# Kernel tuning notes

Measured on AMD Instinct MI355X. Metric: run time of the kernel, lower is better.

Reference implementation:

```python
import jax, jax.numpy as jnp
import numpy as np
import math

NUM_BUCKETS = 32
MAX_DISTANCE = 128
N_HEADS = 16
D_KV = 64


def _relative_position_bucket(relative_position, num_buckets=NUM_BUCKETS, max_distance=MAX_DISTANCE):
    # bidirectional (encoder) variant: is_decoder=False
    nb = num_buckets // 2
    rel_buckets = (relative_position > 0).astype(jnp.int32) * nb
    rp = jnp.abs(relative_position)
    max_exact = nb // 2
    is_small = rp < max_exact
    rp_large = max_exact + (
        jnp.log(rp.astype(jnp.float32) / max_exact)
        / math.log(max_distance / max_exact)
        * (nb - max_exact)
    ).astype(jnp.int32)
    rp_large = jnp.minimum(rp_large, nb - 1)
    return rel_buckets + jnp.where(is_small, rp, rp_large)


def compute_position_bias(rel_bias_table, q_len, k_len):
    ctx = jnp.arange(q_len, dtype=jnp.int32)[:, None]
    mem = jnp.arange(k_len, dtype=jnp.int32)[None, :]
    buckets = _relative_position_bucket(mem - ctx)  # [q_len, k_len]
    values = rel_bias_table[buckets]                # [q_len, k_len, H]
    return jnp.transpose(values, (2, 0, 1))[None]   # [1, H, q_len, k_len]


def setup_inputs() -> dict:
    key = jax.random.key(0)
    ks = jax.random.split(key, 6)
    B, S, D = 2, 2048, 1024
    s = 0.02
    return {
        "hidden_states": jax.random.normal(ks[0], (B, S, D), dtype=jnp.float32),
        "Wq": jax.random.normal(ks[1], (D, N_HEADS * D_KV), dtype=jnp.float32) * s,
        "Wk": jax.random.normal(ks[2], (D, N_HEADS * D_KV), dtype=jnp.float32) * s,
        "Wv": jax.random.normal(ks[3], (D, N_HEADS * D_KV), dtype=jnp.float32) * s,
        "Wo": jax.random.normal(ks[4], (N_HEADS * D_KV, D), dtype=jnp.float32) * s,
        "rel_bias_table": jax.random.normal(ks[5], (NUM_BUCKETS, N_HEADS), dtype=jnp.float32),
    }


def reference(hidden_states, Wq, Wk, Wv, Wo, rel_bias_table):
    B, S, D = hidden_states.shape
    H, dh = N_HEADS, D_KV
    q = (hidden_states @ Wq).reshape(B, S, H, dh)
    k = (hidden_states @ Wk).reshape(B, S, H, dh)
    v = (hidden_states @ Wv).reshape(B, S, H, dh)

    position_bias = compute_position_bias(rel_bias_table, S, S)  # [1,H,S,S]

    scale = 1.0 / math.sqrt(dh)  # applied inside optimized_attention (SDPA convention)
    scores = jnp.einsum('bqhd,bkhd->bhqk', q, k) * scale + position_bias
    probs = jax.nn.softmax(scores, axis=-1)
    ctx = jnp.einsum('bhqk,bkhd->bqhd', probs, v).reshape(B, S, H * dh)
    attn_output = ctx @ Wo
    return attn_output
```

## Files before the change

### kernel.cpp

```cpp
#include <hip/hip_runtime.h>

typedef __attribute__((ext_vector_type(8))) short s16x8;
typedef __attribute__((ext_vector_type(4))) short s16x4;
typedef __attribute__((ext_vector_type(4))) float f32x4;
typedef __attribute__((ext_vector_type(4))) unsigned int u32x4;
typedef __attribute__((ext_vector_type(2))) unsigned int u32x2;
typedef unsigned short u16;
typedef unsigned int u32;

#define LOG2E 1.4426950408889634f

__device__ __forceinline__ u16 f2bf(float x) {
  u32 u = __float_as_uint(x);
  u += 0x7FFFu + ((u >> 16) & 1u);
  return (u16)(u >> 16);
}

__device__ __forceinline__ float bf2f(u16 x) {
  return __uint_as_float((u32)x << 16);
}

__device__ __forceinline__ u32 pack_bf_trunc(float lo, float hi) {
  return (__float_as_uint(lo) >> 16) | (__float_as_uint(hi) & 0xFFFF0000u);
}

__device__ __forceinline__ void gl_lds16(const void* g, void* l) {
  __builtin_amdgcn_global_load_lds((const __attribute__((address_space(1))) void*)g,
                                   (__attribute__((address_space(3))) void*)l, 16, 0, 0);
}

#define MFMA16(a, b, c) __builtin_amdgcn_mfma_f32_16x16x32_bf16((a), (b), (c), 0, 0, 0)


__global__ __launch_bounds__(256) void prep(const float* __restrict__ hs,
                                            const float* __restrict__ Wq,
                                            const float* __restrict__ Wk,
                                            const float* __restrict__ Wv,
                                            const float* __restrict__ Wo,
                                            const float* __restrict__ tbl,
                                            u16* __restrict__ hsb,
                                            u16* __restrict__ wt,
                                            u16* __restrict__ wot,
                                            float* __restrict__ biasT) {
  const int blk = blockIdx.x;
  const int tid = threadIdx.x;
  if (blk < 2048) {
    const int i = blk * 256 + tid;
    const float4* s4 = (const float4*)hs;
    float4 a = s4[i * 2];
    float4 b = s4[i * 2 + 1];
    s16x8 o;
    o[0] = (short)f2bf(a.x); o[1] = (short)f2bf(a.y);
    o[2] = (short)f2bf(a.z); o[3] = (short)f2bf(a.w);
    o[4] = (short)f2bf(b.x); o[5] = (short)f2bf(b.y);
    o[6] = (short)f2bf(b.z); o[7] = (short)f2bf(b.w);
    *(s16x8*)&hsb[i * 8] = o;
  } else if (blk < 4096) {
    int r = blk - 2048;
    const int sel = r >> 9;
    r &= 511;
    const float* W = sel == 0 ? Wq : (sel == 1 ? Wk : (sel == 2 ? Wv : Wo));
    u16* dst = sel == 3 ? wot : wt + sel * 1048576;
    const int n = (r & 15) * 64 + (tid & 63);
    const int kb = (r >> 4) * 32 + (tid >> 6) * 8;
    s16x8 o;
#pragma unroll
    for (int j = 0; j < 8; ++j) o[j] = (short)f2bf(W[(kb + j) * 1024 + n]);
    *(s16x8*)&dst[n * 1024 + kb] = o;
  } else {
    const int i = (blk - 4096) * 256 + tid;
    const int h = i >> 12, dp = i & 4095;
    const int delta = dp - 2047;
    const int rp = delta < 0 ? -delta : delta;
    int bucket = delta > 0 ? 16 : 0;
    if (rp < 8)
      bucket += rp;
    else
      bucket += 8 + (rp >= 12) + (rp >= 16) + (rp >= 23) + (rp >= 32) +
                (rp >= 46) + (rp >= 64) + (rp >= 91);
    biasT[i] = tbl[bucket * 16 + h] * LOG2E;
  }
}


__device__ __forceinline__ void gemm_core(const u16* __restrict__ A,
                                          const u16* __restrict__ Bt,
                                          int m0, int n0,
                                          u16* As, u16* Bs, f32x4 acc[4][4]) {
  const int tid = threadIdx.x;
  const int w = tid >> 6, l = tid & 63, g = l >> 4, m15 = l & 15;
  const int wr = (w >> 1) * 64, wc = (w & 1) * 64;
#pragma unroll
  for (int i = 0; i < 4; ++i)
#pragma unroll
    for (int j = 0; j < 4; ++j) acc[i][j] = (f32x4){0.f, 0.f, 0.f, 0.f};

  for (int kt = 0; kt < 16; ++kt) {
    const int k0 = kt * 64;
    __syncthreads();
#pragma unroll
    for (int c = 0; c < 4; ++c) {
      const int idx = c * 256 + tid;
      const int row = idx >> 3, col16 = idx & 7;
      const int scol = col16 ^ (row & 7);
      gl_lds16(&A[(m0 + row) * 1024 + k0 + scol * 8], (char*)As + c * 4096 + w * 1024);
      gl_lds16(&Bt[(n0 + row) * 1024 + k0 + scol * 8], (char*)Bs + c * 4096 + w * 1024);
    }
    __syncthreads();
#pragma unroll
    for (int ks = 0; ks < 2; ++ks) {
      s16x8 af[4], bf[4];
#pragma unroll
      for (int mf = 0; mf < 4; ++mf) {
        const int row = wr + mf * 16 + m15;
        af[mf] = *(const s16x8*)&As[(row * 8 + ((ks * 4 + g) ^ (row & 7))) * 8];
      }
#pragma unroll
      for (int nf = 0; nf < 4; ++nf) {
        const int row = wc + nf * 16 + m15;
        bf[nf] = *(const s16x8*)&Bs[(row * 8 + ((ks * 4 + g) ^ (row & 7))) * 8];
      }
#pragma unroll
      for (int mf = 0; mf < 4; ++mf)
#pragma unroll
        for (int nf = 0; nf < 4; ++nf)
          acc[mf][nf] = MFMA16(af[mf], bf[nf], acc[mf][nf]);
    }
  }
}

__global__ __launch_bounds__(256) void gemm_qkv(const u16* __restrict__ X,
                                                const u16* __restrict__ Wt,
                                                u16* __restrict__ Q,
                                                u16* __restrict__ Kb,
                                                u16* __restrict__ VT) {
  __shared__ u16 shbuf[16384];
  u16* As = shbuf;
  u16* Bs = shbuf + 8192;
  f32x4 acc[4][4];
  const int flat = blockIdx.x;
  const int x = flat & 7, i = flat >> 3;
  const int m0 = ((x & 3) * 8 + (i & 7)) * 128;
  const int n0 = ((x >> 2) * 12 + (i >> 3)) * 128;
  gemm_core(X, Wt, m0, n0, As, Bs, acc);

  const int tid = threadIdx.x;
  const int w = tid >> 6, l = tid & 63, g = l >> 4, m15 = l & 15;
  const int wr = (w >> 1) * 64, wc = (w & 1) * 64;
  const int nsel = n0 >> 10;
  const int ncol0 = (n0 & 1023) + wc;
  if (nsel == 2) {
    __syncthreads();
#pragma unroll
    for (int mf = 0; mf < 4; ++mf) {
      const int s_base = wr + mf * 16 + g * 4;
#pragma unroll
      for (int nf = 0; nf < 4; ++nf) {
        const int d_loc = wc + nf * 16 + m15;
        s16x4 pk;
#pragma unroll
        for (int r = 0; r < 4; ++r) pk[r] = (short)f2bf(acc[mf][nf][r]);
        *(s16x4*)&shbuf[d_loc * 128 + (s_base ^ ((d_loc & 7) << 3))] = pk;
      }
    }
    __syncthreads();
    const int b = m0 >> 11, sg0 = m0 & 2047;
#pragma unroll
    for (int it = 0; it < 8; ++it) {
      const int d_loc = it * 16 + w * 4 + g;
      const s16x8 v =
          *(const s16x8*)&shbuf[d_loc * 128 + ((m15 * 8) ^ ((d_loc & 7) << 3))];
      const int col = (n0 & 1023) + d_loc;
      *(s16x8*)&VT[((b * 16 + (col >> 6)) * 64 + (col & 63)) * 2048 + sg0 + m15 * 8] = v;
    }
  } else {
    u16* dst = nsel == 0 ? Q : Kb;
    const float scale = nsel == 0 ? 0.125f * LOG2E : 1.0f;
#pragma unroll
    for (int mf = 0; mf < 4; ++mf) {
      const int rbase = m0 + wr + mf * 16 + g * 4;
#pragma unroll
      for (int nf = 0; nf < 4; ++nf) {
        const int col = ncol0 + nf * 16 + m15;
#pragma unroll
        for (int r = 0; r < 4; ++r)
          dst[(rbase + r) * 1024 + col] = f2bf(acc[mf][nf][r] * scale);
      }
    }
  }
}

__global__ __launch_bounds__(256) void gemm_out(const u16* __restrict__ CTX,
                                                const u16* __restrict__ Wot,
                                                float* __restrict__ Out) {
  __shared__ u16 shbuf[16384];
  u16* As = shbuf;
  u16* Bs = shbuf + 8192;
  f32x4 acc[4][4];
  const int flat = blockIdx.x;
  const int x = flat & 7, i = flat >> 3;
  const int m0 = ((x & 3) * 8 + (i & 7)) * 128;
  const int n0 = ((x >> 2) * 4 + (i >> 3)) * 128;
  gemm_core(CTX, Wot, m0, n0, As, Bs, acc);

  const int tid = threadIdx.x;
  const int w = tid >> 6, l = tid & 63, g = l >> 4, m15 = l & 15;
  const int wr = (w >> 1) * 64, wc = (w & 1) * 64;
#pragma unroll
  for (int mf = 0; mf < 4; ++mf) {
    const int rbase = m0 + wr + mf * 16 + g * 4;
#pragma unroll
    for (int nf = 0; nf < 4; ++nf) {
      const int col = n0 + wc + nf * 16 + m15;
#pragma unroll
      for (int r = 0; r < 4; ++r)
        Out[(rbase + r) * 1024 + col] = acc[mf][nf][r];
    }
  }
}


__global__ __launch_bounds__(256, 4) void attn_kernel(const u16* __restrict__ Qg,
                                                      const u16* __restrict__ Kg,
                                                      const u16* __restrict__ VTg,
                                                      const float* __restrict__ biasT,
                                                      const float* __restrict__ tbl,
                                                      u16* __restrict__ po0,
                                                      u16* __restrict__ po1,
                                                      float* __restrict__ pls) {
  __shared__ u16 KT[2][4096];
  __shared__ u16 VTs[2][4096];

  const int tid = threadIdx.x;
  const int w = tid >> 6, l = tid & 63, g = l >> 4, m15 = l & 15;
  const int flat = blockIdx.x;
  const int nf_ = (flat & 7) * 128 + (flat >> 3);
  const int bh = nf_ >> 5;
  const int rem = nf_ & 31;
  const int half = rem >> 4, qblk = rem & 15;
  const int b = bh >> 4, h = bh & 15;
  const int qw = qblk * 128 + w * 32;
  const int kvbase = half * 1024;

  u16* poh = half ? po1 : po0;
  float* plsh = pls + half * 65536;

  const float fpos = tbl[31 * 16 + h] * LOG2E;
  const float fneg = tbl[15 * 16 + h] * LOG2E;

  s16x8 aq[2][2];
#pragma unroll
  for (int qs = 0; qs < 2; ++qs) {
    const u16* qp = &Qg[(b * 2048 + qw + qs * 16 + m15) * 1024 + h * 64 + g * 8];
    aq[qs][0] = *(const s16x8*)qp;
    aq[qs][1] = *(const s16x8*)(qp + 32);
  }

  s16x8 vone;
#pragma unroll
  for (int j = 0; j < 8; ++j) vone[j] = (short)0x3F80;

  f32x4 o[2][4];
  f32x4 ls4[2];
#pragma unroll
  for (int qs = 0; qs < 2; ++qs) {
    ls4[qs] = (f32x4){0.f, 0.f, 0.f, 0.f};
#pragma unroll
    for (int d = 0; d < 4; ++d) o[qs][d] = (f32x4){0.f, 0.f, 0.f, 0.f};
  }

  const u16* Kbase = &Kg[(b * 2048 + kvbase) * 1024 + h * 64];
  const u16* Vbase = &VTg[bh * 64 * 2048 + kvbase];

#define STAGE(buf, kv0)                                                          \
  {                                                                              \
    _Pragma("unroll") for (int c = 0; c < 2; ++c) {                              \
      const int idx = c * 256 + tid;                                             \
      const int row = idx >> 3, col16 = idx & 7;                                 \
      const int scol = col16 ^ (row & 7);                                        \
      gl_lds16(&Kbase[(kv0 + row) * 1024 + scol * 8],                            \
               (char*)KT + (buf)*8192 + c * 4096 + w * 1024);                    \
      gl_lds16(&Vbase[row * 2048 + (kv0) + scol * 8],                            \
               (char*)VTs + (buf)*8192 + c * 4096 + w * 1024);                   \
    }                                                                            \
  }

  STAGE(0, 0);
  int cur = 0;
  for (int t = 0; t < 16; ++t) {
    const int kv0 = t * 64;
    __syncthreads();
    if (t < 15) STAGE(cur ^ 1, kv0 + 64);

    const u16* KTc = &KT[cur][0];
    const u16* VTc = &VTs[cur][0];

    f32x4 s[2][4];
    const int diff = kvbase + kv0 - qw;
    if (diff <= -160 || diff >= 128) {
      const float bc = diff > 0 ? fpos : fneg;
#pragma unroll
      for (int qs = 0; qs < 2; ++qs)
#pragma unroll
        for (int c = 0; c < 4; ++c) s[qs][c] = (f32x4){bc, bc, bc, bc};
    } else {
#pragma unroll
      for (int qs = 0; qs < 2; ++qs) {
        const float* bp =
            &biasT[h * 4096 + kvbase + kv0 + g * 4 - qw - qs * 16 - m15 + 2047];
#pragma unroll
        for (int c = 0; c < 4; ++c)
#pragma unroll
          for (int r = 0; r < 4; ++r) s[qs][c][r] = bp[c * 16 + r];
      }
    }

    __builtin_amdgcn_s_setprio(1);
#pragma unroll
    for (int ks = 0; ks < 2; ++ks) {
#pragma unroll
      for (int c = 0; c < 4; ++c) {
        const int row = c * 16 + m15;
        const s16x8 bk = *(const s16x8*)&KTc[(row * 8 + ((ks * 4 + g) ^ (row & 7))) * 8];
        s[0][c] = MFMA16(bk, aq[0][ks], s[0][c]);
        s[1][c] = MFMA16(bk, aq[1][ks], s[1][c]);
      }
    }
    __builtin_amdgcn_s_setprio(0);

    s16x8 pa[2][2];
#pragma unroll
    for (int qs = 0; qs < 2; ++qs) {
      u32 w01[4], w23[4];
#pragma unroll
      for (int c = 0; c < 4; ++c) {
        w01[c] = pack_bf_trunc(__builtin_amdgcn_exp2f(s[qs][c][0]),
                               __builtin_amdgcn_exp2f(s[qs][c][1]));
        w23[c] = pack_bf_trunc(__builtin_amdgcn_exp2f(s[qs][c][2]),
                               __builtin_amdgcn_exp2f(s[qs][c][3]));
      }
#pragma unroll
      for (int ks = 0; ks < 2; ++ks) {
        u32x2 rA = __builtin_amdgcn_permlane32_swap(w01[2 * ks], w01[2 * ks + 1], false, false);
        u32x2 rB = __builtin_amdgcn_permlane16_swap(rA[0], rA[1], false, false);
        u32x2 rC = __builtin_amdgcn_permlane32_swap(w23[2 * ks], w23[2 * ks + 1], false, false);
        u32x2 rD = __builtin_amdgcn_permlane16_swap(rC[0], rC[1], false, false);
        const u32x4 pd = (u32x4){rB[0], rD[0], rB[1], rD[1]};
        pa[qs][ks] = __builtin_bit_cast(s16x8, pd);
      }
    }

    __builtin_amdgcn_s_setprio(1);
#pragma unroll
    for (int ks = 0; ks < 2; ++ks) {
#pragma unroll
      for (int d = 0; d < 4; ++d) {
        const int rowv = d * 16 + m15;
        const s16x8 bv = *(const s16x8*)&VTc[(rowv * 8 + ((ks * 4 + g) ^ (rowv & 7))) * 8];
        o[0][d] = MFMA16(pa[0][ks], bv, o[0][d]);
        o[1][d] = MFMA16(pa[1][ks], bv, o[1][d]);
      }
      ls4[0] = MFMA16(pa[0][ks], vone, ls4[0]);
      ls4[1] = MFMA16(pa[1][ks], vone, ls4[1]);
    }
    __builtin_amdgcn_s_setprio(0);
    cur ^= 1;
  }
#undef STAGE

#pragma unroll
  for (int qs = 0; qs < 2; ++qs) {
    const int orow = b * 2048 + qw + qs * 16 + g * 4;
    const int ocol = h * 64 + m15;
#pragma unroll
    for (int r = 0; r < 4; ++r) {
#pragma unroll
      for (int d = 0; d < 4; ++d)
        poh[(orow + r) * 1024 + ocol + d * 16] = f2bf(o[qs][d][r]);
      if (m15 == 0) plsh[(orow + r) * 16 + h] = ls4[qs][r];
    }
  }
}

__global__ __launch_bounds__(256) void merge(const u16* __restrict__ po0,
                                             const u16* __restrict__ po1,
                                             const float* __restrict__ pls,
                                             u16* __restrict__ ctx) {
  const int i = blockIdx.x * 256 + threadIdx.x;
  const int row = i >> 7;
  const int seg = i & 127;
  const int h = seg >> 3;
  const float den = 1.0f / (pls[row * 16 + h] + pls[65536 + row * 16 + h]);
  const s16x8 a = *(const s16x8*)&po0[row * 1024 + seg * 8];
  const s16x8 b = *(const s16x8*)&po1[row * 1024 + seg * 8];
  s16x8 o;
#pragma unroll
  for (int j = 0; j < 8; ++j)
    o[j] = (short)f2bf((bf2f((u16)a[j]) + bf2f((u16)b[j])) * den);
  *(s16x8*)&ctx[row * 1024 + seg * 8] = o;
}


extern "C" void kernel_launch(void* const* d_in, const int* in_sizes, int n_in,
                              void* d_out, int out_size, void* d_ws, size_t ws_size,
                              hipStream_t stream) {
  (void)in_sizes; (void)n_in; (void)out_size; (void)ws_size;
  const float* hs  = (const float*)d_in[0];
  const float* Wq  = (const float*)d_in[1];
  const float* Wk  = (const float*)d_in[2];
  const float* Wv  = (const float*)d_in[3];
  const float* Wo  = (const float*)d_in[4];
  const float* tbl = (const float*)d_in[5];

  char* ws = (char*)d_ws;
  u16* hsb   = (u16*)(ws);
  u16* wt    = (u16*)(ws + 8388608);
  u16* wot   = (u16*)(ws + 14680064);
  u16* q     = (u16*)(ws + 16777216);
  u16* k     = (u16*)(ws + 25165824);
  u16* po0   = (u16*)(ws + 33554432);
  u16* vt    = (u16*)(ws + 41943040);
  u16* ctx   = (u16*)(ws + 50331648);
  float* biasT = (float*)(ws + 58720256);
  u16* po1   = hsb;
  float* pls = (float*)wt;

  prep<<<4352, 256, 0, stream>>>(hs, Wq, Wk, Wv, Wo, tbl, hsb, wt, wot, biasT);
  gemm_qkv<<<768, 256, 0, stream>>>(hsb, wt, q, k, vt);
  attn_kernel<<<1024, 256, 0, stream>>>(q, k, vt, biasT, tbl, po0, po1, pls);
  merge<<<2048, 256, 0, stream>>>(po0, po1, pls, ctx);
  gemm_out<<<256, 256, 0, stream>>>(ctx, wot, (float*)d_out);
}
```

Baseline: 127.4 us.

## Double-buffer GEMM LDS tiles with K=32 stages to overlap loads and MFMA

The shared GEMM core used by the QKV and output projections now loads K-slices of 32 into two alternating LDS buffers. The next slice's global-to-LDS copy is issued before computing on the current one, and the second barrier per iteration is removed. The swizzle is adapted to the narrower 4-chunk rows. Halving the K tile doubles the loop iterations and barriers in exchange for overlapping memory latency with compute within the same 32 KB of LDS.

```diff
diff --git a/kernel.cpp b/kernel.cpp
--- a/kernel.cpp
+++ b/kernel.cpp
@@ -86,7 +86,7 @@
 __device__ __forceinline__ void gemm_core(const u16* __restrict__ A,
                                           const u16* __restrict__ Bt,
                                           int m0, int n0,
-                                          u16* As, u16* Bs, f32x4 acc[4][4]) {
+                                          u16* shbuf, f32x4 acc[4][4]) {
   const int tid = threadIdx.x;
   const int w = tid >> 6, l = tid & 63, g = l >> 4, m15 = l & 15;
   const int wr = (w >> 1) * 64, wc = (w & 1) * 64;
@@ -95,38 +95,45 @@
 #pragma unroll
     for (int j = 0; j < 4; ++j) acc[i][j] = (f32x4){0.f, 0.f, 0.f, 0.f};
 
-  for (int kt = 0; kt < 16; ++kt) {
-    const int k0 = kt * 64;
+#define GSTAGE(buf, k0)                                                    \
+  {                                                                        \
+    _Pragma("unroll") for (int c = 0; c < 2; ++c) {                        \
+      const int idx = c * 256 + tid;                                       \
+      const int row = idx >> 2, col4 = idx & 3;                            \
+      const int scol = col4 ^ ((row >> 1) & 3);                            \
+      gl_lds16(&A[(m0 + row) * 1024 + (k0) + scol * 8],                    \
+               (char*)shbuf + (buf)*8192 + c * 4096 + w * 1024);           \
+      gl_lds16(&Bt[(n0 + row) * 1024 + (k0) + scol * 8],                   \
+               (char*)shbuf + 16384 + (buf)*8192 + c * 4096 + w * 1024);   \
+    }                                                                      \
+  }
+
+  GSTAGE(0, 0);
+  int cur = 0;
+  for (int kt = 0; kt < 32; ++kt) {
     __syncthreads();
-#pragma unroll
-    for (int c = 0; c < 4; ++c) {
-      const int idx = c * 256 + tid;
-      const int row = idx >> 3, col16 = idx & 7;
-      const int scol = col16 ^ (row & 7);
-      gl_lds16(&A[(m0 + row) * 1024 + k0 + scol * 8], (char*)As + c * 4096 + w * 1024);
-      gl_lds16(&Bt[(n0 + row) * 1024 + k0 + scol * 8], (char*)Bs + c * 4096 + w * 1024);
-    }
-    __syncthreads();
-#pragma unroll
-    for (int ks = 0; ks < 2; ++ks) {
-      s16x8 af[4], bf[4];
-#pragma unroll
-      for (int mf = 0; mf < 4; ++mf) {
-        const int row = wr + mf * 16 + m15;
-        af[mf] = *(const s16x8*)&As[(row * 8 + ((ks * 4 + g) ^ (row & 7))) * 8];
-      }
-#pragma unroll
-      for (int nf = 0; nf < 4; ++nf) {
-        const int row = wc + nf * 16 + m15;
-        bf[nf] = *(const s16x8*)&Bs[(row * 8 + ((ks * 4 + g) ^ (row & 7))) * 8];
-      }
-#pragma unroll
-      for (int mf = 0; mf < 4; ++mf)
-#pragma unroll
-        for (int nf = 0; nf < 4; ++nf)
-          acc[mf][nf] = MFMA16(af[mf], bf[nf], acc[mf][nf]);
-    }
-  }
+    if (kt < 31) GSTAGE(cur ^ 1, (kt + 1) * 32);
+    const u16* Asb = shbuf + cur * 4096;
+    const u16* Bsb = shbuf + 8192 + cur * 4096;
+    s16x8 af[4], bfr[4];
+#pragma unroll
+    for (int mf = 0; mf < 4; ++mf) {
+      const int row = wr + mf * 16 + m15;
+      af[mf] = *(const s16x8*)&Asb[(row * 4 + (g ^ ((row >> 1) & 3))) * 8];
+    }
+#pragma unroll
+    for (int nf = 0; nf < 4; ++nf) {
+      const int row = wc + nf * 16 + m15;
+      bfr[nf] = *(const s16x8*)&Bsb[(row * 4 + (g ^ ((row >> 1) & 3))) * 8];
+    }
+#pragma unroll
+    for (int mf = 0; mf < 4; ++mf)
+#pragma unroll
+      for (int nf = 0; nf < 4; ++nf)
+        acc[mf][nf] = MFMA16(af[mf], bfr[nf], acc[mf][nf]);
+    cur ^= 1;
+  }
+#undef GSTAGE
 }
 
 __global__ __launch_bounds__(256) void gemm_qkv(const u16* __restrict__ X,
@@ -135,14 +142,12 @@
                                                 u16* __restrict__ Kb,
                                                 u16* __restrict__ VT) {
   __shared__ u16 shbuf[16384];
-  u16* As = shbuf;
-  u16* Bs = shbuf + 8192;
   f32x4 acc[4][4];
   const int flat = blockIdx.x;
   const int x = flat & 7, i = flat >> 3;
   const int m0 = ((x & 3) * 8 + (i & 7)) * 128;
   const int n0 = ((x >> 2) * 12 + (i >> 3)) * 128;
-  gemm_core(X, Wt, m0, n0, As, Bs, acc);
+  gemm_core(X, Wt, m0, n0, shbuf, acc);
 
   const int tid = threadIdx.x;
   const int w = tid >> 6, l = tid & 63, g = l >> 4, m15 = l & 15;
@@ -194,14 +199,12 @@
                                                 const u16* __restrict__ Wot,
                                                 float* __restrict__ Out) {
   __shared__ u16 shbuf[16384];
-  u16* As = shbuf;
-  u16* Bs = shbuf + 8192;
   f32x4 acc[4][4];
   const int flat = blockIdx.x;
   const int x = flat & 7, i = flat >> 3;
   const int m0 = ((x & 3) * 8 + (i & 7)) * 128;
   const int n0 = ((x >> 2) * 4 + (i >> 3)) * 128;
-  gemm_core(CTX, Wot, m0, n0, As, Bs, acc);
+  gemm_core(CTX, Wot, m0, n0, shbuf, acc);
 
   const int tid = threadIdx.x;
   const int w = tid >> 6, l = tid & 63, g = l >> 4, m15 = l & 15;
```

New measurement: 120.7 us. 1.05x faster.
